# Kernel tuning notes

Measured on AMD Instinct MI355X. Metric: run time of the kernel, lower is better.

## Reference

```python
import jax, jax.numpy as jnp
import numpy as np

HEAD_DIM = 64  # dim // num_heads with dim=64, num_heads=1


def _weighted_adj(x):
    # x: [B, N, C] tokens. Faithful translation of Weighted_adj.forward.
    B, N, C = x.shape
    scale = 1.0 / jnp.sqrt(jnp.float32(HEAD_DIM))

    # --- Norm_dynamic_adj: per-sample pairwise distances (torch code loops
    # over B calling scipy cdist / np.corrcoef on CPU; here fully vectorized).
    diff = x[:, :, None, :] - x[:, None, :, :]          # [B, N, N, C]
    adj_euclidean = jnp.sqrt(jnp.sum(diff * diff, axis=-1))  # cdist 'euclidean'
    adj_chebyshev = jnp.max(jnp.abs(diff), axis=-1)          # cdist 'chebyshev'

    # np.corrcoef over rows of x[b]
    xc = x - jnp.mean(x, axis=-1, keepdims=True)
    cov = jnp.einsum('bic,bjc->bij', xc, xc)             # [B, N, N]
    std = jnp.sqrt(jnp.diagonal(cov, axis1=1, axis2=2))  # [B, N]
    adj_corrcoef = jnp.clip(cov / (std[:, :, None] * std[:, None, :]), -1.0, 1.0)

    # --- attention over adjacencies (num_heads=1, so head reshape is identity)
    # q = euclidean, k = chebyshev, v = corrcoef
    attn = jax.nn.softmax(
        jnp.einsum('bik,bjk->bij', adj_euclidean, adj_chebyshev) * scale, axis=-1)
    weighted = jnp.einsum('bij,bjk->bik', attn, adj_corrcoef)  # [B, N, N]

    # --- numpy-style top-k binarization: keep top floor(N*N/6) entries per sample
    S = N * N
    w = weighted.reshape(B, S)
    ranks = jnp.argsort(jnp.argsort(w, axis=1), axis=1)  # argsort(argsort) ranks
    mask = (ranks >= S - S // 6).astype(jnp.float32)
    return mask.reshape(B, N, N)


def setup_inputs() -> dict:
    key = jax.random.key(0)
    x = jax.random.normal(key, (2, 1024, 64), dtype=jnp.float32)
    return {"x": x}


def reference(x):
    return _weighted_adj(x)
```

## Files before the change

kernel.cpp:

```cpp
#include <hip/hip_runtime.h>
#include <hip/hip_bf16.h>

constexpr int BB = 2;
constexpr int N  = 1024;
constexpr int C  = 64;
constexpr int S  = N * N;
constexpr int KSEL = S / 6;
constexpr int EQCAP   = 1 << 17;
constexpr int NSELBLK = 256;

typedef double d4 __attribute__((ext_vector_type(4)));

__device__ __forceinline__ unsigned long long d2key(double d) {
    unsigned long long u = (unsigned long long)__double_as_longlong(d);
    return (u & 0x8000000000000000ULL) ? ~u : (u | 0x8000000000000000ULL);
}

__device__ __forceinline__ unsigned int aload(const unsigned int* p) {
    return __hip_atomic_load(p, __ATOMIC_RELAXED, __HIP_MEMORY_SCOPE_AGENT);
}
__device__ __forceinline__ unsigned long long aload64(const unsigned long long* p) {
    return __hip_atomic_load(p, __ATOMIC_RELAXED, __HIP_MEMORY_SCOPE_AGENT);
}
__device__ __forceinline__ void astore64(unsigned long long* p, unsigned long long v) {
    (void)__hip_atomic_exchange(p, v, __ATOMIC_RELAXED, __HIP_MEMORY_SCOPE_AGENT);
}

__device__ __forceinline__ void xcd_tile(int& i0, int& j0) {
    int lin = (int)blockIdx.x + 32 * (int)blockIdx.y;
    int xcd = lin & 7, idx = lin >> 3;
    int nby = (xcd >> 1) * 4 + (idx >> 4);
    int nbx = (xcd & 1) * 16 + (idx & 15);
    i0 = nby * 64; j0 = nbx * 32;
}

__device__ __forceinline__ void pick256(unsigned int c, unsigned int kneed,
                                        int t, unsigned int* wsum,
                                        unsigned int* s_bk, unsigned int* s_ca) {
    int lane = t & 63, wv = t >> 6;
    unsigned int ws = c;
#pragma unroll
    for (int off = 1; off < 64; off <<= 1) {
        unsigned int o = __shfl_down(ws, off);
        if (lane + off < 64) ws += o;
    }
    if (lane == 0) wsum[wv] = ws;
    __syncthreads();
    unsigned int add = 0;
#pragma unroll
    for (int w2 = 1; w2 < 4; ++w2) if (w2 > wv) add += wsum[w2];
    unsigned int S_t = ws + add, S_nx = S_t - c;
    if (S_t >= kneed && S_nx < kneed) { *s_bk = (unsigned int)t; *s_ca = S_nx; }
    __syncthreads();
}

__global__ __launch_bounds__(256) void k_pairwise(const float* __restrict__ x,
                                                  double* __restrict__ E,
                                                  double* __restrict__ Ch,
                                                  double* __restrict__ Cc) {
    int b  = blockIdx.z;
    int i0 = blockIdx.y * 64;
    int j0 = blockIdx.x * 64;
    __shared__ double xi[64][65];
    __shared__ double xj[64][65];
    __shared__ double mi[64], ri_[64], si[64];
    __shared__ double mj[64], rj_[64], sj[64];

    int t  = threadIdx.x;
    int r  = t >> 2;
    int cb = (t & 3) * 16;
    const float* xb = x + (size_t)b * N * C;
    {
        const float4* pi = (const float4*)(xb + (size_t)(i0 + r) * C + cb);
        const float4* pj = (const float4*)(xb + (size_t)(j0 + r) * C + cb);
#pragma unroll
        for (int m4 = 0; m4 < 4; ++m4) {
            float4 fi = pi[m4], fj = pj[m4];
            xi[r][cb + 4 * m4 + 0] = (double)fi.x; xi[r][cb + 4 * m4 + 1] = (double)fi.y;
            xi[r][cb + 4 * m4 + 2] = (double)fi.z; xi[r][cb + 4 * m4 + 3] = (double)fi.w;
            xj[r][cb + 4 * m4 + 0] = (double)fj.x; xj[r][cb + 4 * m4 + 1] = (double)fj.y;
            xj[r][cb + 4 * m4 + 2] = (double)fj.z; xj[r][cb + 4 * m4 + 3] = (double)fj.w;
        }
    }
    __syncthreads();

    if (t < 128) {
        int row = t & 63;
        const double (*xs)[65] = (t < 64) ? xi : xj;
        double sum = 0.0, rr = 0.0;
#pragma unroll 8
        for (int c = 0; c < 64; ++c) { double v = xs[row][c]; sum += v; rr = fma(v, v, rr); }
        double m = sum / 64.0;
        double q = 0.0;
#pragma unroll 8
        for (int c = 0; c < 64; ++c) { double w = xs[row][c] - m; q = fma(w, w, q); }
        double sv = 1.0 / sqrt(q);
        if (t < 64) { mi[row] = m; ri_[row] = rr; si[row] = sv; }
        else        { mj[row] = m; rj_[row] = rr; sj[row] = sv; }
    }
    __syncthreads();

    int ty = t >> 4, tx = t & 15;
    double adot[4][4] = {};
    double amax[4][4] = {};
#pragma unroll 8
    for (int c = 0; c < 64; ++c) {
        double ai[4], aj[4];
#pragma unroll
        for (int p = 0; p < 4; ++p) ai[p] = xi[ty + 16 * p][c];
#pragma unroll
        for (int q = 0; q < 4; ++q) aj[q] = xj[tx + 16 * q][c];
#pragma unroll
        for (int p = 0; p < 4; ++p)
#pragma unroll
            for (int q = 0; q < 4; ++q) {
                double d = ai[p] - aj[q];
                amax[p][q] = fmax(amax[p][q], fabs(d));
                adot[p][q] = fma(ai[p], aj[q], adot[p][q]);
            }
    }

#pragma unroll
    for (int p = 0; p < 4; ++p) {
        int li = ty + 16 * p;
        int ii = i0 + li;
        double rri = ri_[li], mmi = mi[li], ssi = si[li];
#pragma unroll
        for (int q = 0; q < 4; ++q) {
            int lj = tx + 16 * q;
            int jj = j0 + lj;
            double dot = adot[p][q];
            double d2  = rri + rj_[lj] - 2.0 * dot;
            double e   = (ii == jj) ? 0.0 : sqrt(fmax(d2, 0.0));
            double cc  = (dot - 64.0 * mmi * mj[lj]) * ssi * sj[lj];
            cc = fmin(1.0, fmax(-1.0, cc));
            size_t idx = (size_t)b * S + (size_t)ii * N + jj;
            E[idx]  = e;
            Ch[idx] = amax[p][q];
            Cc[idx] = cc;
        }
    }
}

__global__ __launch_bounds__(256, 4) void k_gemm_nt(const double* __restrict__ A,
                                                    const double* __restrict__ Bm,
                                                    double* __restrict__ Cm,
                                                    double scale,
                                                    unsigned int* __restrict__ bar,
                                                    unsigned int* __restrict__ ghist,
                                                    unsigned int* __restrict__ eqcnt,
                                                    unsigned long long* __restrict__ pubR) {
    if (blockIdx.x == 0 && blockIdx.y == 0 && blockIdx.z == 0) {
        int tt = threadIdx.x;
        for (int i = tt; i < 512; i += 256) bar[i] = 0u;
        for (int i = tt; i < 4 * 2 * 16 * 256; i += 256) ghist[i] = 0u;
        if (tt < 32) eqcnt[tt] = 0u;
        if (tt < 16) { pubR[tt] = 0ULL; }
    }

    int b = blockIdx.z;
    const double* Ab = A  + (size_t)b * S;
    const double* Bb = Bm + (size_t)b * S;
    double*       Cb = Cm + (size_t)b * S;
    int i0, j0;
    xcd_tile(i0, j0);

    __shared__ double At[2][64][17];
    __shared__ double Bt[2][32][17];

    int t    = threadIdx.x;
    int lane = t & 63;
    int w    = t >> 6;
    int wrr  = w * 16;
    int fm   = lane & 15;
    int fk   = lane >> 4;

    int sa_r = t >> 2, sa_c = (t & 3) * 4;
    int sb_r = t >> 3, sb_c = (t & 7) * 2;

    d4 acc0 = {0.0, 0.0, 0.0, 0.0};
    d4 acc1 = acc0;

    const double* ap = Ab + (size_t)(i0 + sa_r) * N + sa_c;
    const double* bp = Bb + (size_t)(j0 + sb_r) * N + sb_c;

    double pa[4], pb[2];
#pragma unroll
    for (int m = 0; m < 4; ++m) pa[m] = ap[m];
#pragma unroll
    for (int m = 0; m < 2; ++m) pb[m] = bp[m];
#pragma unroll
    for (int m = 0; m < 4; ++m) At[0][sa_r][sa_c + m] = pa[m];
#pragma unroll
    for (int m = 0; m < 2; ++m) Bt[0][sb_r][sb_c + m] = pb[m];
    __syncthreads();

    int cur = 0;
    for (int k0 = 0; k0 < N; k0 += 16) {
        bool has_next = (k0 + 16 < N);
        if (has_next) {
            ap += 16; bp += 16;
#pragma unroll
            for (int m = 0; m < 4; ++m) pa[m] = ap[m];
#pragma unroll
            for (int m = 0; m < 2; ++m) pb[m] = bp[m];
        }
#pragma unroll
        for (int kq = 0; kq < 4; ++kq) {
            int kk = kq * 4 + fk;
            double a0 = At[cur][wrr + fm][kk];
            double b0 = Bt[cur][fm][kk];
            double b1 = Bt[cur][16 + fm][kk];
            acc0 = __builtin_amdgcn_mfma_f64_16x16x4f64(a0, b0, acc0, 0, 0, 0);
            acc1 = __builtin_amdgcn_mfma_f64_16x16x4f64(a0, b1, acc1, 0, 0, 0);
        }
        if (has_next) {
            int nxt = cur ^ 1;
#pragma unroll
            for (int m = 0; m < 4; ++m) At[nxt][sa_r][sa_c + m] = pa[m];
#pragma unroll
            for (int m = 0; m < 2; ++m) Bt[nxt][sb_r][sb_c + m] = pb[m];
            __syncthreads();
            cur = nxt;
        }
    }
    int r0 = i0 + wrr + 4 * fk;
    int c0 = j0 + fm;
#pragma unroll
    for (int r = 0; r < 4; ++r) {
        Cb[(size_t)(r0 + r) * N + c0]      = acc0[r] * scale;
        Cb[(size_t)(r0 + r) * N + c0 + 16] = acc1[r] * scale;
    }
}

__global__ __launch_bounds__(256, 4) void k_gemm_nn(const double* __restrict__ A,
                                                    const double* __restrict__ Bm,
                                                    double* __restrict__ Wm,
                                                    unsigned int* __restrict__ kq_out,
                                                    unsigned int* __restrict__ ghist) {
    int b = blockIdx.z;
    const double* Ab = A  + (size_t)b * S;
    const double* Bb = Bm + (size_t)b * S;
    double*       Wb = Wm + (size_t)b * S;
    unsigned int* kb = kq_out + (size_t)b * S;
    int i0, j0;
    xcd_tile(i0, j0);

    __shared__ double At[2][64][17];
    __shared__ double Bt[2][16][33];
    __shared__ int bh[256];

    int t    = threadIdx.x;
    int lane = t & 63;
    int w    = t >> 6;
    int wrr  = w * 16;
    int fm   = lane & 15;
    int fk   = lane >> 4;

    int sa_r = t >> 2, sa_c = (t & 3) * 4;
    int sb_r = t >> 4, sb_c = (t & 15) * 2;

    d4 acc0 = {0.0, 0.0, 0.0, 0.0};
    d4 acc1 = acc0;

    const double* ap = Ab + (size_t)(i0 + sa_r) * N + sa_c;
    const double* bp = Bb + (size_t)sb_r * N + j0 + sb_c;

    double pa[4], pb[2];
#pragma unroll
    for (int m = 0; m < 4; ++m) pa[m] = ap[m];
#pragma unroll
    for (int m = 0; m < 2; ++m) pb[m] = bp[m];
#pragma unroll
    for (int m = 0; m < 4; ++m) At[0][sa_r][sa_c + m] = pa[m];
#pragma unroll
    for (int m = 0; m < 2; ++m) Bt[0][sb_r][sb_c + m] = pb[m];
    __syncthreads();

    int cur = 0;
    for (int k0 = 0; k0 < N; k0 += 16) {
        bool has_next = (k0 + 16 < N);
        if (has_next) {
            ap += 16; bp += (size_t)16 * N;
#pragma unroll
            for (int m = 0; m < 4; ++m) pa[m] = ap[m];
#pragma unroll
            for (int m = 0; m < 2; ++m) pb[m] = bp[m];
        }
#pragma unroll
        for (int kq = 0; kq < 4; ++kq) {
            int kk = kq * 4 + fk;
            double a0 = At[cur][wrr + fm][kk];
            double b0 = Bt[cur][kk][fm];
            double b1 = Bt[cur][kk][16 + fm];
            acc0 = __builtin_amdgcn_mfma_f64_16x16x4f64(a0, b0, acc0, 0, 0, 0);
            acc1 = __builtin_amdgcn_mfma_f64_16x16x4f64(a0, b1, acc1, 0, 0, 0);
        }
        if (has_next) {
            int nxt = cur ^ 1;
#pragma unroll
            for (int m = 0; m < 4; ++m) At[nxt][sa_r][sa_c + m] = pa[m];
#pragma unroll
            for (int m = 0; m < 2; ++m) Bt[nxt][sb_r][sb_c + m] = pb[m];
            __syncthreads();
            cur = nxt;
        }
    }
    int r0 = i0 + wrr + 4 * fk;
    int c0 = j0 + fm;

    unsigned int kreg[8];
#pragma unroll
    for (int r = 0; r < 4; ++r) {
        double w00 = acc0[r], w01 = acc1[r];
        size_t i00 = (size_t)(r0 + r) * N + c0;
        size_t i01 = (size_t)(r0 + r) * N + c0 + 16;
        unsigned int k00 = (unsigned int)(d2key(w00) >> 32);
        unsigned int k01 = (unsigned int)(d2key(w01) >> 32);
        Wb[i00] = w00; kb[i00] = k00;
        Wb[i01] = w01; kb[i01] = k01;
        kreg[2 * r + 0] = k00; kreg[2 * r + 1] = k01;
    }

    bh[t] = 0;
    __syncthreads();
#pragma unroll
    for (int m = 0; m < 8; ++m) atomicAdd(&bh[kreg[m] >> 24], 1);
    __syncthreads();
    if (bh[t] != 0)
        __hip_atomic_fetch_add(&ghist[((0 * 2 + b) * 16 + (blockIdx.x & 15)) * 256 + t],
                               (unsigned int)bh[t], __ATOMIC_RELAXED,
                               __HIP_MEMORY_SCOPE_AGENT);
}

__global__ __launch_bounds__(256) void k_softmax(double* __restrict__ L) {
    int row = (blockIdx.x << 2) + (threadIdx.x >> 6);
    int ln  = threadIdx.x & 63;
    double* p = L + (size_t)row * N;

    double v[16];
#pragma unroll
    for (int q = 0; q < 16; ++q) v[q] = p[ln + 64 * q];

    double mx = v[0];
#pragma unroll
    for (int q = 1; q < 16; ++q) mx = fmax(mx, v[q]);
#pragma unroll
    for (int off = 32; off >= 1; off >>= 1) mx = fmax(mx, __shfl_xor(mx, off));

    double s = 0.0;
#pragma unroll
    for (int q = 0; q < 16; ++q) { v[q] = exp(v[q] - mx); s += v[q]; }
#pragma unroll
    for (int off = 32; off >= 1; off >>= 1) s += __shfl_xor(s, off);

    double inv = 1.0 / s;
#pragma unroll
    for (int q = 0; q < 16; ++q) p[ln + 64 * q] = v[q] * inv;
}

__global__ __launch_bounds__(256) void k_select(const unsigned int* __restrict__ key32,
                                                const double* __restrict__ W,
                                                unsigned int* __restrict__ ghist,
                                                unsigned int* __restrict__ eqcnt,
                                                unsigned long long* __restrict__ cand,
                                                unsigned long long* __restrict__ pubR,
                                                unsigned int* __restrict__ bar,
                                                float* __restrict__ out) {
    int blk = blockIdx.x, t = threadIdx.x;
    int b  = blk >> 7;
    int lb = blk & 127;
    int lane = t & 63, wv = t >> 6;
    bool leader = (lb == 0);

    __shared__ int lh[256];
    __shared__ int wtot[4];
    __shared__ unsigned int wsum[4];
    __shared__ unsigned int sbase, s_tot, s_bk, s_ca;
    __shared__ unsigned long long s_pub;

    int r8 = blk & 7;
    int o  = lb >> 3;
    int tf0 = r8 + 16 * o;
    int tf1 = tf0 + 8;
    int rr = t >> 2, c16 = (t & 3) * 16;
    int tb[2];
    tb[0] = ((tf0 >> 4) * 64 + rr) * N + (tf0 & 15) * 64 + c16;
    tb[1] = ((tf1 >> 4) * 64 + rr) * N + (tf1 & 15) * 64 + c16;

    const unsigned int* kb = key32 + (size_t)b * S;
    const double*       Wb = W     + (size_t)b * S;
    unsigned long long* myPubR = &pubR[b * 8];
    unsigned int* arr = bar + 64;

    unsigned int pref = 0, kneed = (unsigned int)KSEL;

    for (int p = 0; p < 4; ++p) {
        int shift = 24 - 8 * p;
        if (p > 0) {
            lh[t] = 0;
            __syncthreads();
#pragma unroll
            for (int u = 0; u < 2; ++u)
#pragma unroll
                for (int m4 = 0; m4 < 4; ++m4) {
                    uint4 kv = *(const uint4*)(kb + tb[u] + 4 * m4);
                    unsigned int ks[4] = {kv.x, kv.y, kv.z, kv.w};
#pragma unroll
                    for (int c = 0; c < 4; ++c) {
                        bool match = (((unsigned long long)(ks[c] ^ pref)) >> (shift + 8)) == 0ULL;
                        if (match) atomicAdd(&lh[(ks[c] >> shift) & 255u], 1);
                    }
                }
            __syncthreads();
            if (lh[t] != 0)
                __hip_atomic_fetch_add(&ghist[((p * 2 + b) * 16 + (lb >> 3)) * 256 + t],
                                       (unsigned int)lh[t], __ATOMIC_RELAXED,
                                       __HIP_MEMORY_SCOPE_AGENT);
            asm volatile("s_waitcnt vmcnt(0)" ::: "memory");
            __syncthreads();
            if (t == 0) {
                unsigned int* slot = &arr[((p - 1) * 2 + b) * 16];
                __hip_atomic_fetch_add(slot, 1u, __ATOMIC_RELAXED,
                                       __HIP_MEMORY_SCOPE_AGENT);
                while (aload(slot) < 128u) __builtin_amdgcn_s_sleep(4);
            }
            __syncthreads();
        }
        unsigned int c = 0;
#pragma unroll
        for (int g = 0; g < 16; ++g)
            c += aload(&ghist[((p * 2 + b) * 16 + g) * 256 + t]);
        pick256(c, kneed, t, wsum, &s_bk, &s_ca);
        pref |= (s_bk << shift);
        kneed -= s_ca;
    }

    unsigned long long lmask = (1ULL << lane) - 1ULL;
    unsigned long long* cb = cand + (size_t)b * EQCAP;
    {
        int wcnt = 0;
#pragma unroll
        for (int u = 0; u < 2; ++u)
#pragma unroll
            for (int m4 = 0; m4 < 4; ++m4) {
                uint4 kv = *(const uint4*)(kb + tb[u] + 4 * m4);
                unsigned int ks[4] = {kv.x, kv.y, kv.z, kv.w};
#pragma unroll
                for (int c = 0; c < 4; ++c) {
                    unsigned long long mb = __ballot(ks[c] == pref);
                    wcnt += (int)__popcll(mb);
                }
            }
        if (lane == 0) wtot[wv] = wcnt;
        __syncthreads();
        if (t == 0) {
            int tot = wtot[0] + wtot[1] + wtot[2] + wtot[3];
            s_tot = (unsigned int)tot;
            sbase = (tot > 0)
                ? __hip_atomic_fetch_add(&eqcnt[b * 16], (unsigned int)tot,
                                         __ATOMIC_RELAXED, __HIP_MEMORY_SCOPE_AGENT)
                : 0u;
        }
        __syncthreads();
        unsigned int wb2 = sbase;
        for (int w2 = 0; w2 < wv; ++w2) wb2 += (unsigned int)wtot[w2];
#pragma unroll
        for (int u = 0; u < 2; ++u)
#pragma unroll
            for (int m4 = 0; m4 < 4; ++m4) {
                uint4 kv = *(const uint4*)(kb + tb[u] + 4 * m4);
                unsigned int ks[4] = {kv.x, kv.y, kv.z, kv.w};
#pragma unroll
                for (int c = 0; c < 4; ++c) {
                    bool m = (ks[c] == pref);
                    unsigned long long mb = __ballot(m);
                    if (m) {
                        unsigned int pos = wb2 + (unsigned int)__popcll(mb & lmask);
                        if (pos < (unsigned int)EQCAP) {
                            int s = tb[u] + 4 * m4 + c;
                            unsigned int low = (unsigned int)d2key(Wb[s]);
                            astore64(&cb[pos],
                                     (((unsigned long long)(unsigned int)s) << 32) | low);
                        }
                    }
                    wb2 += (unsigned int)__popcll(mb);
                }
            }
    }
    asm volatile("s_waitcnt vmcnt(0)" ::: "memory");
    __syncthreads();
    if (t == 0)
        __hip_atomic_fetch_add(&arr[(6 + b) * 16], 1u,
                               __ATOMIC_RELAXED, __HIP_MEMORY_SCOPE_AGENT);
    unsigned int tot = s_tot;

    float4* ob = (float4*)(out + (size_t)b * S);
#pragma unroll
    for (int u = 0; u < 2; ++u)
#pragma unroll
        for (int m4 = 0; m4 < 4; ++m4) {
            uint4 kv = *(const uint4*)(kb + tb[u] + 4 * m4);
            unsigned int ks[4] = {kv.x, kv.y, kv.z, kv.w};
            float4 ov;
            ov.x = (ks[0] > pref) ? 1.0f : 0.0f;
            ov.y = (ks[1] > pref) ? 1.0f : 0.0f;
            ov.z = (ks[2] > pref) ? 1.0f : 0.0f;
            ov.w = (ks[3] > pref) ? 1.0f : 0.0f;
            ob[(tb[u] >> 2) + m4] = ov;
        }

    if (leader) {
        if (t == 0)
            while (aload(&arr[(6 + b) * 16]) < 128u) __builtin_amdgcn_s_sleep(4);
        __syncthreads();
        unsigned int cnt = aload(&eqcnt[b * 16]);
        if (cnt > (unsigned int)EQCAP) cnt = EQCAP;
        unsigned int rpref = 0, rkneed = kneed;
        for (int shift = 24; shift >= 0; shift -= 8) {
            lh[t] = 0;
            __syncthreads();
            for (unsigned int e = t; e < cnt; e += 256) {
                unsigned int low = (unsigned int)aload64(&cb[e]);
                if ((((unsigned long long)(low ^ rpref)) >> (shift + 8)) == 0ULL)
                    atomicAdd(&lh[(low >> shift) & 255u], 1);
            }
            __syncthreads();
            pick256((unsigned int)lh[t], rkneed, t, wsum, &s_bk, &s_ca);
            rpref |= (s_bk << shift);
            rkneed -= s_ca;
        }
        unsigned int TL = rpref;
        unsigned int ipref = 0;
        for (int shift = 16; shift >= 0; shift -= 8) {
            lh[t] = 0;
            __syncthreads();
            for (unsigned int e = t; e < cnt; e += 256) {
                unsigned long long pr = aload64(&cb[e]);
                if ((unsigned int)pr != TL) continue;
                unsigned int idx = (unsigned int)(pr >> 32);
                if ((((unsigned long long)(idx ^ ipref)) >> (shift + 8)) == 0ULL)
                    atomicAdd(&lh[(idx >> shift) & 255u], 1);
            }
            __syncthreads();
            pick256((unsigned int)lh[t], rkneed, t, wsum, &s_bk, &s_ca);
            ipref |= (s_bk << shift);
            rkneed -= s_ca;
        }
        if (t == 0)
            astore64(myPubR, (1ULL << 56) | (((unsigned long long)TL) << 20) |
                             (unsigned long long)ipref);
    } else if (tot == 0) {
        return;
    }
    if (tot == 0) return;

    if (t == 0) {
        unsigned long long v;
        while (((v = aload64(myPubR)) >> 56) != 1ULL) __builtin_amdgcn_s_sleep(4);
        s_pub = v;
    }
    __syncthreads();
    unsigned long long vR = s_pub;
    unsigned int TL   = (unsigned int)((vR >> 20) & 0xFFFFFFFFULL);
    unsigned int sCut = (unsigned int)(vR & 0xFFFFFULL);

    asm volatile("s_waitcnt vmcnt(0)" ::: "memory");
    float* of = out + (size_t)b * S;
#pragma unroll
    for (int u = 0; u < 2; ++u)
#pragma unroll
        for (int m4 = 0; m4 < 4; ++m4) {
            uint4 kv = *(const uint4*)(kb + tb[u] + 4 * m4);
            unsigned int ks[4] = {kv.x, kv.y, kv.z, kv.w};
#pragma unroll
            for (int c = 0; c < 4; ++c) {
                if (ks[c] == pref) {
                    int s = tb[u] + 4 * m4 + c;
                    unsigned int low = (unsigned int)d2key(Wb[s]);
                    of[s] = (low > TL || (low == TL && (unsigned int)s >= sCut))
                                ? 1.0f : 0.0f;
                }
            }
        }
}

extern "C" void kernel_launch(void* const* d_in, const int* in_sizes, int n_in,
                              void* d_out, int out_size, void* d_ws, size_t ws_size,
                              hipStream_t stream) {
    const float* x = (const float*)d_in[0];
    float* out = (float*)d_out;

    char* ws = (char*)d_ws;
    size_t off = 0;
    auto alloc = [&](size_t bytes) -> void* {
        void* p = ws + off;
        off += (bytes + 255) & ~(size_t)255;
        return p;
    };

    double* E     = (double*)alloc((size_t)BB * S * sizeof(double));
    double* Ch    = (double*)alloc((size_t)BB * S * sizeof(double));
    double* Cc    = (double*)alloc((size_t)BB * S * sizeof(double));
    double* L     = (double*)alloc((size_t)BB * S * sizeof(double));
    unsigned int* key32 = (unsigned int*)alloc((size_t)BB * S * sizeof(unsigned int));
    double* W     = E;
    unsigned int* bar   = (unsigned int*)alloc(2048);
    unsigned int* ghist = (unsigned int*)alloc(4 * 2 * 16 * 256 * sizeof(unsigned int));
    unsigned int* eqcnt = (unsigned int*)alloc(BB * 64);
    unsigned long long* cand =
        (unsigned long long*)alloc((size_t)BB * EQCAP * sizeof(unsigned long long));
    unsigned long long* pubR = (unsigned long long*)alloc(128);

    k_pairwise<<<dim3(N / 64, N / 64, BB), 256, 0, stream>>>(x, E, Ch, Cc);

    k_gemm_nt<<<dim3(N / 32, N / 64, BB), 256, 0, stream>>>(E, Ch, L, 0.125,
                                                            bar, ghist, eqcnt, pubR);

    k_softmax<<<512, 256, 0, stream>>>(L);

    k_gemm_nn<<<dim3(N / 32, N / 64, BB), 256, 0, stream>>>(L, Cc, W, key32, ghist);

    k_select<<<NSELBLK, 256, 0, stream>>>(key32, W, ghist, eqcnt, cand, pubR, bar, out);
}
```

Baseline: 282.6 us.

## Exit radix-select passes early once pivot bucket is small enough

```diff
diff --git a/kernel.cpp b/kernel.cpp
--- a/kernel.cpp
+++ b/kernel.cpp
@@ -8,6 +8,7 @@
 constexpr int KSEL = S / 6;
 constexpr int EQCAP   = 1 << 17;
 constexpr int NSELBLK = 256;
+constexpr unsigned int HEXIT = 16384;
 
 typedef double d4 __attribute__((ext_vector_type(4)));
 
@@ -36,7 +37,8 @@
 
 __device__ __forceinline__ void pick256(unsigned int c, unsigned int kneed,
                                         int t, unsigned int* wsum,
-                                        unsigned int* s_bk, unsigned int* s_ca) {
+                                        unsigned int* s_bk, unsigned int* s_ca,
+                                        unsigned int* s_hc) {
     int lane = t & 63, wv = t >> 6;
     unsigned int ws = c;
 #pragma unroll
@@ -50,7 +52,9 @@
 #pragma unroll
     for (int w2 = 1; w2 < 4; ++w2) if (w2 > wv) add += wsum[w2];
     unsigned int S_t = ws + add, S_nx = S_t - c;
-    if (S_t >= kneed && S_nx < kneed) { *s_bk = (unsigned int)t; *s_ca = S_nx; }
+    if (S_t >= kneed && S_nx < kneed) {
+        *s_bk = (unsigned int)t; *s_ca = S_nx; *s_hc = c;
+    }
     __syncthreads();
 }
 
@@ -363,7 +367,8 @@
                                                 const double* __restrict__ W,
                                                 unsigned int* __restrict__ ghist,
                                                 unsigned int* __restrict__ eqcnt,
-                                                unsigned long long* __restrict__ cand,
+                                                unsigned long long* __restrict__ candA,
+                                                unsigned long long* __restrict__ candB,
                                                 unsigned long long* __restrict__ pubR,
                                                 unsigned int* __restrict__ bar,
                                                 float* __restrict__ out) {
@@ -376,8 +381,8 @@
     __shared__ int lh[256];
     __shared__ int wtot[4];
     __shared__ unsigned int wsum[4];
-    __shared__ unsigned int sbase, s_tot, s_bk, s_ca;
-    __shared__ unsigned long long s_pub;
+    __shared__ unsigned int sbase, s_tot, s_bk, s_ca, s_hc;
+    __shared__ unsigned long long s_pub, s_pub2;
 
     int r8 = blk & 7;
     int o  = lb >> 3;
@@ -390,10 +395,12 @@
 
     const unsigned int* kb = key32 + (size_t)b * S;
     const double*       Wb = W     + (size_t)b * S;
-    unsigned long long* myPubR = &pubR[b * 8];
+    unsigned long long* cA = candA + (size_t)b * EQCAP;
+    unsigned long long* cB = candB + (size_t)b * EQCAP;
     unsigned int* arr = bar + 64;
 
     unsigned int pref = 0, kneed = (unsigned int)KSEL;
+    int plen = 8;
 
     for (int p = 0; p < 4; ++p) {
         int shift = 24 - 8 * p;
@@ -431,13 +438,16 @@
 #pragma unroll
         for (int g = 0; g < 16; ++g)
             c += aload(&ghist[((p * 2 + b) * 16 + g) * 256 + t]);
-        pick256(c, kneed, t, wsum, &s_bk, &s_ca);
+        pick256(c, kneed, t, wsum, &s_bk, &s_ca, &s_hc);
         pref |= (s_bk << shift);
         kneed -= s_ca;
-    }
+        plen = 8 * (p + 1);
+        if (p == 3 || s_hc <= HEXIT) break;
+    }
+    int rsh = 32 - plen;
+    unsigned int prefv = pref >> rsh;
 
     unsigned long long lmask = (1ULL << lane) - 1ULL;
-    unsigned long long* cb = cand + (size_t)b * EQCAP;
     {
         int wcnt = 0;
 #pragma unroll
@@ -448,7 +458,7 @@
                 unsigned int ks[4] = {kv.x, kv.y, kv.z, kv.w};
 #pragma unroll
                 for (int c = 0; c < 4; ++c) {
-                    unsigned long long mb = __ballot(ks[c] == pref);
+                    unsigned long long mb = __ballot(((ks[c] ^ pref) >> rsh) == 0);
                     wcnt += (int)__popcll(mb);
                 }
             }
@@ -473,15 +483,14 @@
                 unsigned int ks[4] = {kv.x, kv.y, kv.z, kv.w};
 #pragma unroll
                 for (int c = 0; c < 4; ++c) {
-                    bool m = (ks[c] == pref);
+                    bool m = ((ks[c] ^ pref) >> rsh) == 0;
                     unsigned long long mb = __ballot(m);
                     if (m) {
                         unsigned int pos = wb2 + (unsigned int)__popcll(mb & lmask);
                         if (pos < (unsigned int)EQCAP) {
                             int s = tb[u] + 4 * m4 + c;
-                            unsigned int low = (unsigned int)d2key(Wb[s]);
-                            astore64(&cb[pos],
-                                     (((unsigned long long)(unsigned int)s) << 32) | low);
+                            astore64(&cA[pos], d2key(Wb[s]));
+                            astore64(&cB[pos], (unsigned long long)(unsigned int)s);
                         }
                     }
                     wb2 += (unsigned int)__popcll(mb);
@@ -503,10 +512,10 @@
             uint4 kv = *(const uint4*)(kb + tb[u] + 4 * m4);
             unsigned int ks[4] = {kv.x, kv.y, kv.z, kv.w};
             float4 ov;
-            ov.x = (ks[0] > pref) ? 1.0f : 0.0f;
-            ov.y = (ks[1] > pref) ? 1.0f : 0.0f;
-            ov.z = (ks[2] > pref) ? 1.0f : 0.0f;
-            ov.w = (ks[3] > pref) ? 1.0f : 0.0f;
+            ov.x = ((ks[0] >> rsh) > prefv) ? 1.0f : 0.0f;
+            ov.y = ((ks[1] >> rsh) > prefv) ? 1.0f : 0.0f;
+            ov.z = ((ks[2] >> rsh) > prefv) ? 1.0f : 0.0f;
+            ov.w = ((ks[3] >> rsh) > prefv) ? 1.0f : 0.0f;
             ob[(tb[u] >> 2) + m4] = ov;
         }
 
@@ -516,54 +525,61 @@
         __syncthreads();
         unsigned int cnt = aload(&eqcnt[b * 16]);
         if (cnt > (unsigned int)EQCAP) cnt = EQCAP;
-        unsigned int rpref = 0, rkneed = kneed;
-        for (int shift = 24; shift >= 0; shift -= 8) {
+        unsigned long long rpref = ((unsigned long long)pref) << 32;
+        unsigned int rkneed = kneed;
+        for (int shift = 24 + rsh; shift >= 0; shift -= 8) {
             lh[t] = 0;
             __syncthreads();
             for (unsigned int e = t; e < cnt; e += 256) {
-                unsigned int low = (unsigned int)aload64(&cb[e]);
-                if ((((unsigned long long)(low ^ rpref)) >> (shift + 8)) == 0ULL)
-                    atomicAdd(&lh[(low >> shift) & 255u], 1);
+                unsigned long long k64 = aload64(&cA[e]);
+                if (((k64 ^ rpref) >> (shift + 8)) == 0ULL)
+                    atomicAdd(&lh[(unsigned int)((k64 >> shift) & 255ULL)], 1);
             }
             __syncthreads();
-            pick256((unsigned int)lh[t], rkneed, t, wsum, &s_bk, &s_ca);
-            rpref |= (s_bk << shift);
+            pick256((unsigned int)lh[t], rkneed, t, wsum, &s_bk, &s_ca, &s_hc);
+            rpref |= ((unsigned long long)s_bk) << shift;
             rkneed -= s_ca;
         }
-        unsigned int TL = rpref;
+        unsigned long long TL64 = rpref;
         unsigned int ipref = 0;
         for (int shift = 16; shift >= 0; shift -= 8) {
             lh[t] = 0;
             __syncthreads();
             for (unsigned int e = t; e < cnt; e += 256) {
-                unsigned long long pr = aload64(&cb[e]);
-                if ((unsigned int)pr != TL) continue;
-                unsigned int idx = (unsigned int)(pr >> 32);
+                unsigned long long k64 = aload64(&cA[e]);
+                if (k64 != TL64) continue;
+                unsigned int idx = (unsigned int)aload64(&cB[e]);
                 if ((((unsigned long long)(idx ^ ipref)) >> (shift + 8)) == 0ULL)
                     atomicAdd(&lh[(idx >> shift) & 255u], 1);
             }
             __syncthreads();
-            pick256((unsigned int)lh[t], rkneed, t, wsum, &s_bk, &s_ca);
+            pick256((unsigned int)lh[t], rkneed, t, wsum, &s_bk, &s_ca, &s_hc);
             ipref |= (s_bk << shift);
             rkneed -= s_ca;
         }
-        if (t == 0)
-            astore64(myPubR, (1ULL << 56) | (((unsigned long long)TL) << 20) |
-                             (unsigned long long)ipref);
+        if (t == 0) {
+            astore64(&pubR[b * 8 + 1], (1ULL << 56) | (TL64 & 0xFFFFFFFFULL));
+            astore64(&pubR[b * 8],
+                     (1ULL << 56) | (((unsigned long long)ipref) << 32) | (TL64 >> 32));
+        }
     } else if (tot == 0) {
         return;
     }
     if (tot == 0) return;
 
     if (t == 0) {
-        unsigned long long v;
-        while (((v = aload64(myPubR)) >> 56) != 1ULL) __builtin_amdgcn_s_sleep(4);
-        s_pub = v;
-    }
-    __syncthreads();
-    unsigned long long vR = s_pub;
-    unsigned int TL   = (unsigned int)((vR >> 20) & 0xFFFFFFFFULL);
-    unsigned int sCut = (unsigned int)(vR & 0xFFFFFULL);
+        unsigned long long v0, v1;
+        for (;;) {
+            v0 = aload64(&pubR[b * 8]);
+            v1 = aload64(&pubR[b * 8 + 1]);
+            if ((v0 >> 56) == 1ULL && (v1 >> 56) == 1ULL) break;
+            __builtin_amdgcn_s_sleep(4);
+        }
+        s_pub = v0; s_pub2 = v1;
+    }
+    __syncthreads();
+    unsigned long long TL64 = ((s_pub & 0xFFFFFFFFULL) << 32) | (s_pub2 & 0xFFFFFFFFULL);
+    unsigned int sCut = (unsigned int)((s_pub >> 32) & 0xFFFFFULL);
 
     asm volatile("s_waitcnt vmcnt(0)" ::: "memory");
     float* of = out + (size_t)b * S;
@@ -575,10 +591,10 @@
             unsigned int ks[4] = {kv.x, kv.y, kv.z, kv.w};
 #pragma unroll
             for (int c = 0; c < 4; ++c) {
-                if (ks[c] == pref) {
+                if (((ks[c] ^ pref) >> rsh) == 0) {
                     int s = tb[u] + 4 * m4 + c;
-                    unsigned int low = (unsigned int)d2key(Wb[s]);
-                    of[s] = (low > TL || (low == TL && (unsigned int)s >= sCut))
+                    unsigned long long k64 = d2key(Wb[s]);
+                    of[s] = (k64 > TL64 || (k64 == TL64 && (unsigned int)s >= sCut))
                                 ? 1.0f : 0.0f;
                 }
             }
@@ -608,7 +624,9 @@
     unsigned int* bar   = (unsigned int*)alloc(2048);
     unsigned int* ghist = (unsigned int*)alloc(4 * 2 * 16 * 256 * sizeof(unsigned int));
     unsigned int* eqcnt = (unsigned int*)alloc(BB * 64);
-    unsigned long long* cand =
+    unsigned long long* candA =
+        (unsigned long long*)alloc((size_t)BB * EQCAP * sizeof(unsigned long long));
+    unsigned long long* candB =
         (unsigned long long*)alloc((size_t)BB * EQCAP * sizeof(unsigned long long));
     unsigned long long* pubR = (unsigned long long*)alloc(128);
 
@@ -621,5 +639,6 @@
 
     k_gemm_nn<<<dim3(N / 32, N / 64, BB), 256, 0, stream>>>(L, Cc, W, key32, ghist);
 
-    k_select<<<NSELBLK, 256, 0, stream>>>(key32, W, ghist, eqcnt, cand, pubR, bar, out);
-}
+    k_select<<<NSELBLK, 256, 0, stream>>>(key32, W, ghist, eqcnt, candA, candB,
+                                          pubR, bar, out);
+}
```

Result: slower. 321.2 us (+13.6%).
